# Kernel optimization log

Measured on AMD Instinct MI355X. Metric: run time of the kernel, lower is better.

## Reference

```python
import jax, jax.numpy as jnp
import numpy as np

B, C_IN, H, W = 2, 256, 48, 48
OC, G, KH, KW, PH, PW = 256, 4, 7, 7, 3, 3


def _patches(y, Hn, Wn):
    # y: (B, C, Hp, Wp) -> (B, C, KH, KW, Hn, Wn); stride=1, dilation=1
    return jnp.stack([
        jnp.stack([y[:, :, i:i + Hn, j:j + Wn] for j in range(KW)], axis=2)
        for i in range(KH)
    ], axis=2)


def setup_inputs() -> dict:
    key = jax.random.key(0)
    k1, k2, k3, k4 = jax.random.split(key, 4)
    fan_out = 3 * OC  # 1x1 conv, kaiming fan_out
    conv_w = jax.random.normal(k2, (3 * OC, C_IN), dtype=jnp.float32) * np.sqrt(2.0 / fan_out).astype(np.float32)
    return {
        "x": jax.random.normal(k1, (B, C_IN, H, W), dtype=jnp.float32),
        "conv_w": conv_w,
        "rpe_h": jax.random.normal(k3, (G, 1, KH, 1, (OC // G) // 2), dtype=jnp.float32),
        "rpe_w": jax.random.normal(k4, (G, 1, 1, KW, (OC // G) // 2), dtype=jnp.float32),
    }


def reference(x, conv_w, rpe_h, rpe_w):
    b, c, h, w = x.shape
    goc = OC // G
    c2 = goc // 2
    K = KH * KW
    center = (K - 1) // 2
    ci, cj = center // KW, center % KW

    # 1x1 conv to 3*OC channels, then zero-pad (equiv. to Conv2d(padding) + bias=False)
    y = jnp.einsum('bchw,oc->bohw', x, conv_w)
    y = jnp.pad(y, ((0, 0), (0, 0), (PH, PH), (PW, PW)))
    Hn = h + 2 * PH - (KH - 1)
    Wn = w + 2 * PW - (KW - 1)
    P = Hn * Wn

    q_full, k_full, v_full = jnp.split(y, 3, axis=1)

    # query: only the center element of each window is used
    query = q_full[:, :, ci:ci + Hn, cj:cj + Wn].reshape(b, G, goc, P)
    query = jnp.transpose(query, (0, 1, 3, 2))  # (B,G,P,goc)

    # key: full windows + relative position embeddings
    kp = _patches(k_full, Hn, Wn).reshape(b, G, goc, KH, KW, P)
    key = jnp.transpose(kp, (0, 1, 5, 3, 4, 2))  # (B,G,P,KH,KW,goc)
    key = jnp.concatenate((key[..., :c2] + rpe_h, key[..., c2:] + rpe_w), axis=1)  # (B,2G,P,KH,KW,c2)
    key = key.reshape(b, G, P, K, goc)  # row-major reshape matches torch

    vp = _patches(v_full, Hn, Wn).reshape(b, G, goc, K, P)
    value = jnp.transpose(vp, (0, 1, 4, 3, 2))  # (B,G,P,K,goc)

    att = jax.nn.softmax(jnp.einsum('bgpc,bgpkc->bgpk', query, key), axis=-1)
    out = jnp.einsum('bgpk,bgpkc->bgpc', att, value)  # (B,G,P,goc)
    out = jnp.transpose(out, (0, 1, 3, 2)).reshape(b, OC, Hn, Wn)
    return out
```

## Files before the change

kernel.cpp:

```cpp
#include <hip/hip_runtime.h>

#define BB   2
#define CIN  256
#define OC3  768
#define NG   4
#define GOC  64
#define C2   32
#define KK   49
#define PP   2304
#define HALF_P 1152

#define RS      56
#define BROWS   54
#define BSTRIDE (BROWS * RS * OC3)
#define IOFF    ((3 * RS + 3) * OC3)

#define Y2_BYTES  (BB * BROWS * RS * OC3 * 4)
#define XT_OFF    Y2_BYTES
#define WT_OFF    (XT_OFF + BB * PP * 512 * 2)

typedef __attribute__((ext_vector_type(8))) short bf16x8;
typedef __attribute__((ext_vector_type(4))) float f32x4;

static __device__ __forceinline__ unsigned short f2bf_rne(float x) {
    unsigned int u = __float_as_uint(x);
    unsigned int r = u + 0x7FFFu + ((u >> 16) & 1u);
    return (unsigned short)(r >> 16);
}
static __device__ __forceinline__ float bf2f(unsigned short h) {
    return __uint_as_float(((unsigned int)h) << 16);
}

template <int C>
static __device__ __forceinline__ float dppf(float x) {
    return __int_as_float(__builtin_amdgcn_update_dpp(
        0, __float_as_int(x), C, 0xF, 0xF, true));
}
template <int D>
static __device__ __forceinline__ float xor_lane(float x) {
    if constexpr (D == 1)       return dppf<0xB1>(x);
    else if constexpr (D == 2)  return dppf<0x4E>(x);
    else if constexpr (D == 4)  return dppf<0x141>(dppf<0x4E>(dppf<0xB1>(x)));
    else if constexpr (D == 8)  return dppf<0x128>(x);
    else                        return __shfl_xor(x, D, 64);
}
template <int N> struct IC { static constexpr int value = N; };

#define ROW4  (RS * OC3 / 4)
#define REG1  (6 * ROW4)
#define COLS4 (OC3 / 4)

__global__ __launch_bounds__(256) void prep(
    float* __restrict__ Y2,
    const float* __restrict__ W, short* __restrict__ Wt,
    const float* __restrict__ X, short* __restrict__ Xt)
{
    __shared__ float tile[64][65];
    const int bid = blockIdx.x;
    const int t   = threadIdx.x;

    if (bid < 1080) {
        const int idx = (bid % 540) * 256 + t;
        const int b   = bid / 540;
        float4* Yb = (float4*)(Y2 + (size_t)b * BSTRIDE);
        const float4 z = make_float4(0.f, 0.f, 0.f, 0.f);
        if (idx < REG1) {
            int r6  = idx / ROW4;
            int rem = idx - r6 * ROW4;
            int r   = (r6 < 3) ? r6 : 48 + r6;
            Yb[r * ROW4 + rem] = z;
        } else {
            int i2  = idx - REG1;
            int r   = 3 + i2 / (8 * COLS4);
            int rem = i2 - (r - 3) * (8 * COLS4);
            int cg  = rem / COLS4;
            int c   = (cg < 3) ? cg : 48 + cg;
            int ch4 = rem - cg * COLS4;
            Yb[(r * RS + c) * COLS4 + ch4] = z;
        }
    } else if (bid < 1848) {
        int tt = (bid - 1080) * 256 + t;
        int o = tt >> 8, c = tt & 255;
        float v = W[tt];
        unsigned short hi = f2bf_rne(v);
        unsigned short lo = f2bf_rne(v - bf2f(hi));
        Wt[(size_t)o * 512 + c]       = (short)hi;
        Wt[(size_t)o * 512 + 256 + c] = (short)lo;
    } else {
        const int blk = bid - 1848;
        const int p0  = (blk % 36) * 64;
        const int c0  = ((blk / 36) & 3) * 64;
        const int b   = blk / 144;

        const float* Xb = X + (size_t)b * CIN * PP;
        #pragma unroll
        for (int r = 0; r < 16; ++r) {
            int idx = r * 256 + t;
            int c = idx >> 6, p = idx & 63;
            tile[c][p] = Xb[(size_t)(c0 + c) * PP + p0 + p];
        }
        __syncthreads();
        short* Xo = Xt + (size_t)b * PP * 512;
        #pragma unroll
        for (int r = 0; r < 16; ++r) {
            int idx = r * 256 + t;
            int p = idx >> 6, c = idx & 63;
            float v = tile[c][p];
            unsigned short hi = f2bf_rne(v);
            unsigned short lo = f2bf_rne(v - bf2f(hi));
            size_t base = (size_t)(p0 + p) * 512 + c0 + c;
            Xo[base]       = (short)hi;
            Xo[base + 256] = (short)lo;
        }
    }
}

#define LDA 40

__global__ __launch_bounds__(256, 4) void conv_mfma(
    const short* __restrict__ Wt,
    const short* __restrict__ Xt,
    float* __restrict__ Y2)
{
    __shared__ short As[64 * LDA];
    __shared__ short Bs[64 * LDA];

    const int tid = threadIdx.x;
    const int bn  = blockIdx.x;
    const int bm  = blockIdx.y;
    const int b   = blockIdx.z;
    const int om0 = bm * 64, pn0 = bn * 64;

    const int lane = tid & 63, w = tid >> 6;
    const int oq = (w & 1) * 32, pq = (w >> 1) * 32;
    const int ln15 = lane & 15, q = lane >> 4;

    const int  lrow  = (tid & 127) >> 1;
    const int  lsoff = (tid & 1) * 16;
    const bool isA   = tid < 128;
    const short* gA = Wt + (size_t)(om0 + lrow) * 512 + lsoff;
    const short* gB = Xt + (size_t)b * PP * 512 + (size_t)(pn0 + lrow) * 512 + lsoff;
    const short* gsrc = isA ? gA : gB;
    short* ldst = (isA ? As : Bs) + lrow * LDA + lsoff;

    f32x4 acc[2][2] = {};

    for (int k0 = 0; k0 < 768; k0 += 32) {
        const int wk = (k0 < 256) ? k0 : k0 - 256;
        const int xk = (k0 < 512) ? k0 : k0 - 512;
        const int kk = isA ? wk : xk;
        uint4 v0 = *(const uint4*)(gsrc + kk);
        uint4 v1 = *(const uint4*)(gsrc + kk + 8);
        __syncthreads();
        *(uint4*)ldst       = v0;
        *(uint4*)(ldst + 8) = v1;
        __syncthreads();

        bf16x8 af[2], bf[2];
        #pragma unroll
        for (int i = 0; i < 2; ++i) {
            af[i] = *(const bf16x8*)&As[(oq + i * 16 + ln15) * LDA + q * 8];
            bf[i] = *(const bf16x8*)&Bs[(pq + i * 16 + ln15) * LDA + q * 8];
        }
        #pragma unroll
        for (int i = 0; i < 2; ++i)
            #pragma unroll
            for (int j = 0; j < 2; ++j)
                acc[i][j] = __builtin_amdgcn_mfma_f32_16x16x32_bf16(
                    af[i], bf[j], acc[i][j], 0, 0, 0);
    }

    float* Yb = Y2 + (size_t)b * BSTRIDE + IOFF;
    #pragma unroll
    for (int i = 0; i < 2; ++i) {
        #pragma unroll
        for (int j = 0; j < 2; ++j) {
            int o = om0 + oq + i * 16 + q * 4;
            int p = pn0 + pq + j * 16 + ln15;
            int h = p / 48, ww = p - h * 48;
            *(f32x4*)&Yb[(size_t)(h * RS + ww) * OC3 + o] = acc[i][j];
        }
    }
}

struct TagH { static constexpr bool value = true;  };
struct TagW { static constexpr bool value = false; };

__global__ __launch_bounds__(256, 6) void attn_kernel(
    const float* __restrict__ Y2,
    const float* __restrict__ rpe_h,
    const float* __restrict__ rpe_w,
    float* __restrict__ out)
{
    __shared__ float xpose[4][65];

    const int tid  = threadIdx.x;
    const int lane = tid & 63;
    const int w    = tid >> 6;
    const int bx     = blockIdx.x;
    const int wblock = (bx & 7) * 576 + (bx >> 3);
    const int wid    = wblock * 4 + w;
    const int pq   = wid % PP;
    const int g    = (wid / PP) & (NG - 1);
    const int b    = wid / (PP * NG);
    const int ph   = pq / 48;
    const int pw   = pq - ph * 48;

    const float* Yb = Y2 + (size_t)b * BSTRIDE + IOFF;

    const float qv = Yb[(size_t)(ph * RS + pw) * OC3 + g * GOC + lane];

    const int t   = (pq >= HALF_P) ? 1 : 0;
    const int qpr = pq - t * HALF_P;
    const int p0  = 2 * qpr;
    const int ph0 = p0 / 48;
    const int pw0 = p0 - ph0 * 48;
    const int g2  = 2 * g + t;
    const bool use_h = (g2 < NG);
    const int  kch   = use_h ? (CIN + g2 * GOC) : (CIN + (g2 - NG) * GOC + C2);
    const float* rb  = use_h ? (rpe_h + g2 * 7 * C2) : (rpe_w + (g2 - NG) * 7 * C2);

    const int  c  = lane & 31;
    const bool hi = (lane >= 32);

    const float R0 = rb[0 * C2 + c], R1 = rb[1 * C2 + c], R2 = rb[2 * C2 + c],
                R3 = rb[3 * C2 + c], R4 = rb[4 * C2 + c], R5 = rb[5 * C2 + c],
                R6 = rb[6 * C2 + c];

    const float* kb = Yb + (size_t)(ph0 * RS + pw0) * OC3 + kch + c;

    auto rget = [&](int idx) -> float {
        return idx == 0 ? R0 : idx == 1 ? R1 : idx == 2 ? R2 :
               idx == 3 ? R3 : idx == 4 ? R4 : idx == 5 ? R5 : R6;
    };

    auto tree = [&](auto tag) -> float {
        constexpr bool UH = decltype(tag)::value;
        auto chunkprod = [&](int l) -> float {
            int m0 = 2 * l,     h10 = (m0 >= KK), k0 = m0 - KK * h10;
            int m1 = 2 * l + 1, h11 = (m1 >= KK), k1 = m1 - KK * h11;
            int i0 = k0 / 7, j0 = k0 % 7, i1 = k1 / 7, j1 = k1 % 7;
            int d0 = ((i0 - 3) * RS + (h10 + j0 - 3)) * OC3;
            int d1 = ((i1 - 3) * RS + (h11 + j1 - 3)) * OC3;
            float kv = kb[hi ? d1 : d0];
            float ra = UH ? rget(i0) : rget(j0);
            float rc = UH ? rget(i1) : rget(j1);
            kv += hi ? rc : ra;
            return qv * kv;
        };
        auto val = [&](int jj) -> float {
            if (2 * jj >= KK) return 0.f;
            float pa = chunkprod(2 * jj);
            float pb = (2 * jj + 1 < KK) ? chunkprod(2 * jj + 1) : 0.f;
            float u  = (lane & 1) ? pb : pa;
            float ww = (lane & 1) ? pa : pb;
            return u + xor_lane<1>(ww);
        };
        auto comb = [&](auto dc, float x, float y) -> float {
            constexpr int d = decltype(dc)::value;
            float u  = (lane & d) ? y : x;
            float ww = (lane & d) ? x : y;
            return u + xor_lane<d>(ww);
        };
        float acc32[2];
        #pragma unroll
        for (int a = 0; a < 2; ++a) {
            float acc16[2];
            #pragma unroll
            for (int bq = 0; bq < 2; ++bq) {
                float acc8[2];
                #pragma unroll
                for (int cq = 0; cq < 2; ++cq) {
                    float acc4[2];
                    #pragma unroll
                    for (int dq = 0; dq < 2; ++dq) {
                        float acc2[2];
                        #pragma unroll
                        for (int eq = 0; eq < 2; ++eq)
                            acc2[eq] = val(a * 16 + bq * 8 + cq * 4 + dq * 2 + eq);
                        acc4[dq] = comb(IC<2>{}, acc2[0], acc2[1]);
                    }
                    acc8[cq] = comb(IC<4>{}, acc4[0], acc4[1]);
                }
                acc16[bq] = comb(IC<8>{}, acc8[0], acc8[1]);
            }
            acc32[a] = comb(IC<16>{}, acc16[0], acc16[1]);
        }
        return comb(IC<32>{}, acc32[0], acc32[1]);
    };

    const float logit = use_h ? tree(TagH{}) : tree(TagW{});

    float mx = logit;
    mx = fmaxf(mx, xor_lane<1>(mx));
    mx = fmaxf(mx, xor_lane<2>(mx));
    mx = fmaxf(mx, xor_lane<4>(mx));
    mx = fmaxf(mx, xor_lane<8>(mx));
    mx = fmaxf(mx, xor_lane<16>(mx));
    mx = fmaxf(mx, xor_lane<32>(mx));
    float e = (lane < KK) ? __expf(logit - mx) : 0.f;
    float ssum = e;
    ssum += xor_lane<1>(ssum);
    ssum += xor_lane<2>(ssum);
    ssum += xor_lane<4>(ssum);
    ssum += xor_lane<8>(ssum);
    ssum += xor_lane<16>(ssum);
    ssum += xor_lane<32>(ssum);
    const float att = e / ssum;

    float acc = 0.f;
    const float* vb = Yb + (size_t)(ph * RS + pw) * OC3 + 2 * CIN + g * GOC + lane;
    #pragma unroll
    for (int k = 0; k < KK; ++k) {
        int i = k / 7, j = k % 7;
        int doff = ((i - 3) * RS + (j - 3)) * OC3;
        float ak = __uint_as_float(
            __builtin_amdgcn_readlane(__float_as_uint(att), k));
        acc = fmaf(ak, vb[doff], acc);
    }

    xpose[w][lane] = acc;
    __syncthreads();
    const int wid0 = wblock * 4;
    const int pq0  = wid0 % PP;
    const int g0   = (wid0 / PP) & (NG - 1);
    const int b0   = wid0 / (PP * NG);
    const int ch   = tid >> 2;
    const int w2   = tid & 3;
    out[((size_t)b0 * 256 + g0 * GOC + ch) * PP + pq0 + w2] = xpose[w2][ch];
}

extern "C" void kernel_launch(void* const* d_in, const int* in_sizes, int n_in,
                              void* d_out, int out_size, void* d_ws, size_t ws_size,
                              hipStream_t stream)
{
    const float* x  = (const float*)d_in[0];
    const float* w  = (const float*)d_in[1];
    const float* rh = (const float*)d_in[2];
    const float* rw = (const float*)d_in[3];

    float* Y2 = (float*)d_ws;
    short* Xt = (short*)((char*)d_ws + XT_OFF);
    short* Wt = (short*)((char*)d_ws + WT_OFF);

    prep<<<2136, 256, 0, stream>>>(Y2, w, Wt, x, Xt);
    conv_mfma<<<dim3(36, 12, BB), 256, 0, stream>>>(Wt, Xt, Y2);
    attn_kernel<<<(BB * NG * PP) / 4, 256, 0, stream>>>(Y2, rh, rw, (float*)d_out);
}
```

Before: 112.3 us.

## Vectorize attention-value accumulation with float4 loads split across lane quads

The value accumulation no longer has each lane load one scalar channel for all 49 window positions. Each lane now handles 4 channels with float4 loads, and the 4 lanes of a quad split the window positions between them. Attention weights are delivered by ds_swizzle plus a cross-half xor shuffle, and partial sums are reduced within the quad by xor shuffles. This cuts the number of load instructions and readlanes per wave, at the cost of extra shuffles, a divergent tail step, and more complex lane indexing that relies on the `hi` variable defined earlier.

```diff
diff --git a/kernel.cpp b/kernel.cpp
--- a/kernel.cpp
+++ b/kernel.cpp
@@ -185,6 +185,10 @@
 
 struct TagH { static constexpr bool value = true;  };
 struct TagW { static constexpr bool value = false; };
+
+static __host__ __device__ constexpr int vdoff(int t) {
+    return ((t / 7 - 3) * RS + (t % 7 - 3)) * OC3;
+}
 
 __global__ __launch_bounds__(256, 6) void attn_kernel(
     const float* __restrict__ Y2,
@@ -270,17 +274,17 @@
             for (int bq = 0; bq < 2; ++bq) {
                 float acc8[2];
                 #pragma unroll
-                for (int cq = 0; cq < 2; ++cq) {
-                    float acc4[2];
+                for (int cq2 = 0; cq2 < 2; ++cq2) {
+                    float acc4t[2];
                     #pragma unroll
                     for (int dq = 0; dq < 2; ++dq) {
                         float acc2[2];
                         #pragma unroll
                         for (int eq = 0; eq < 2; ++eq)
-                            acc2[eq] = val(a * 16 + bq * 8 + cq * 4 + dq * 2 + eq);
-                        acc4[dq] = comb(IC<2>{}, acc2[0], acc2[1]);
+                            acc2[eq] = val(a * 16 + bq * 8 + cq2 * 4 + dq * 2 + eq);
+                        acc4t[dq] = comb(IC<2>{}, acc2[0], acc2[1]);
                     }
-                    acc8[cq] = comb(IC<4>{}, acc4[0], acc4[1]);
+                    acc8[cq2] = comb(IC<4>{}, acc4t[0], acc4t[1]);
                 }
                 acc16[bq] = comb(IC<8>{}, acc8[0], acc8[1]);
             }
@@ -308,18 +312,60 @@
     ssum += xor_lane<32>(ssum);
     const float att = e / ssum;
 
-    float acc = 0.f;
-    const float* vb = Yb + (size_t)(ph * RS + pw) * OC3 + 2 * CIN + g * GOC + lane;
+    const float attB = __shfl_xor(att, 32, 64);
+    const int  cq = lane >> 2;
+    const int  tq = lane & 3;
+    const bool tq0 = (lane & 1) != 0;
+    const bool tq1 = (lane & 2) != 0;
+
+    const float* vbase = Yb + (size_t)(ph * RS + pw) * OC3 + 2 * CIN + g * GOC + 4 * cq;
+
+    f32x4 acc4 = {0.f, 0.f, 0.f, 0.f};
+
+    auto attw = [&](auto jc) -> float {
+        constexpr int j = decltype(jc)::value;
+        constexpr int OFF = (((4 * j) & 31) << 5) | 0x03;
+        float src = (hi ^ (j >= 8)) ? attB : att;
+        return __int_as_float(__builtin_amdgcn_ds_swizzle(__float_as_int(src), OFF));
+    };
+
+    auto vstep = [&](auto jc) {
+        constexpr int j = decltype(jc)::value;
+        int d01 = tq0 ? vdoff(4 * j + 1) : vdoff(4 * j + 0);
+        int d23 = tq0 ? vdoff(4 * j + 3) : vdoff(4 * j + 2);
+        int dof = tq1 ? d23 : d01;
+        const f32x4 v4 = *(const f32x4*)(vbase + dof);
+        float aj = attw(jc);
+        #pragma unroll
+        for (int cc = 0; cc < 4; ++cc)
+            acc4[cc] = fmaf(aj, v4[cc], acc4[cc]);
+    };
+
+    vstep(IC<0>{});  vstep(IC<1>{});  vstep(IC<2>{});  vstep(IC<3>{});
+    vstep(IC<4>{});  vstep(IC<5>{});  vstep(IC<6>{});  vstep(IC<7>{});
+    vstep(IC<8>{});  vstep(IC<9>{});  vstep(IC<10>{}); vstep(IC<11>{});
+
+    {
+        float aj = attw(IC<12>{});
+        if (tq == 0) {
+            const f32x4 v4 = *(const f32x4*)(vbase + vdoff(48));
+            #pragma unroll
+            for (int cc = 0; cc < 4; ++cc)
+                acc4[cc] = fmaf(aj, v4[cc], acc4[cc]);
+        }
+    }
+
     #pragma unroll
-    for (int k = 0; k < KK; ++k) {
-        int i = k / 7, j = k % 7;
-        int doff = ((i - 3) * RS + (j - 3)) * OC3;
-        float ak = __uint_as_float(
-            __builtin_amdgcn_readlane(__float_as_uint(att), k));
-        acc = fmaf(ak, vb[doff], acc);
-    }
-
-    xpose[w][lane] = acc;
+    for (int cc = 0; cc < 4; ++cc) {
+        float v = acc4[cc];
+        v += xor_lane<1>(v);
+        v += xor_lane<2>(v);
+        acc4[cc] = v;
+    }
+
+    float outv = tq1 ? (tq0 ? acc4[3] : acc4[2]) : (tq0 ? acc4[1] : acc4[0]);
+
+    xpose[w][lane] = outv;
     __syncthreads();
     const int wid0 = wblock * 4;
     const int pq0  = wid0 % PP;
```

Result: slower. 127.6 us (+13.7%).
